# Kernel optimization log

Hardware: AMD Instinct MI355X
Metric: run time of the kernel (lower is better)

The kernel has to match this reference:

```python
import jax, jax.numpy as jnp
import numpy as np

B, IN_DIM, HV_DIM, NUM_CLASSES = 16384, 2048, 8192, 1000


def setup_inputs() -> dict:
    key = jax.random.key(0)
    kx, kp, kc = jax.random.split(key, 3)
    x = jax.random.normal(kx, (B, IN_DIM), dtype=jnp.float32)
    # +/-1 random projection and class hypervectors (2*bernoulli - 1), as in the torch buffers
    proj = (jax.random.randint(kp, (IN_DIM, HV_DIM), 0, 2) * 2 - 1).astype(jnp.float32)
    class_hv = (jax.random.randint(kc, (HV_DIM, NUM_CLASSES), 0, 2) * 2 - 1).astype(jnp.float32)
    return {"x": x, "proj": proj, "class_hv": class_hv}


def reference(x, proj, class_hv):
    # dense projection -> sign binarize -> binary associative-memory matmul (score_mode='dot')
    hv = x @ proj                                   # [B, HV_DIM]
    hv_bin = jnp.where(hv >= 0, 1.0, -1.0).astype(hv.dtype)
    scores = hv_bin @ class_hv                      # [B, NUM_CLASSES]
    return scores, hv_bin
```

## Files before the change

kernel.cpp:

```cpp
#include <hip/hip_runtime.h>
#include <hip/hip_bf16.h>

typedef _Float16 half8  __attribute__((ext_vector_type(8)));
typedef _Float16 half4_t __attribute__((ext_vector_type(4)));
typedef float    floatx4 __attribute__((ext_vector_type(4)));
typedef int      intx4   __attribute__((ext_vector_type(4)));

#define B_DIM   16384
#define IN_D    2048
#define HV_D    8192
#define NC      1000
#define NCP     1024
#define SCORES_N (B_DIM * NC)

#define GLD16(gp, lp) __builtin_amdgcn_global_load_lds( \
    (const __attribute__((address_space(1))) void*)(gp), \
    (__attribute__((address_space(3))) void*)(lp), 16, 0, 0)

__global__ void k_split(const float* __restrict__ x, _Float16* __restrict__ xh) {
    size_t i = (size_t)blockIdx.x * 256 + threadIdx.x;
    floatx4 v = ((const floatx4*)x)[i];
    half4_t h;
#pragma unroll
    for (int j = 0; j < 4; ++j) h[j] = (_Float16)v[j];
    ((half4_t*)xh)[i] = h;
}

__global__ void k_transpose_proj(const float* __restrict__ p, _Float16* __restrict__ pT) {
    __shared__ float tile[64][65];
    const int t = threadIdx.x;
    const int nt = blockIdx.x * 64;
    const int kt = blockIdx.y * 64;
    const int tr = t >> 4, tc = (t & 15) * 4;
#pragma unroll
    for (int s = 0; s < 4; ++s) {
        int r = tr + s * 16;
        floatx4 v = *(const floatx4*)&p[(size_t)(kt + r) * HV_D + nt + tc];
        tile[r][tc] = v[0]; tile[r][tc + 1] = v[1];
        tile[r][tc + 2] = v[2]; tile[r][tc + 3] = v[3];
    }
    __syncthreads();
#pragma unroll
    for (int s = 0; s < 4; ++s) {
        int rn = tr + s * 16;
        half4_t o;
#pragma unroll
        for (int j = 0; j < 4; ++j) o[j] = (_Float16)tile[tc + j][rn];
        *(half4_t*)&pT[(size_t)(nt + rn) * IN_D + kt + tc] = o;
    }
}

__global__ void k_pack_class(const float* __restrict__ c, signed char* __restrict__ cT) {
    __shared__ signed char tile[64][68];
    const int t = threadIdx.x;
    const int nt = blockIdx.x * 64;
    const int kt = blockIdx.y * 64;
    const int nl = t & 63;
    const int n = nt + nl;
#pragma unroll
    for (int s = 0; s < 16; ++s) {
        const int kl = s * 4 + (t >> 6);
        signed char v = 0;
        if (n < NC) {
            float f = c[(size_t)(kt + kl) * NC + n];
            v = (f >= 0.f) ? (signed char)1 : (signed char)-1;
        }
        tile[kl][nl] = v;
    }
    __syncthreads();
    const int wn = t >> 2;
    const int wk = (t & 3) * 16;
    intx4 o;
    signed char* ob = (signed char*)&o;
#pragma unroll
    for (int j = 0; j < 16; ++j) ob[j] = tile[wk + j][wn];
    *(intx4*)&cT[(size_t)(nt + wn) * HV_D + kt + wk] = o;
}

__launch_bounds__(256, 2)
__global__ void k_gemm1(const _Float16* __restrict__ xh,
                        const _Float16* __restrict__ pT,
                        float* __restrict__ hv_out, signed char* __restrict__ hvb,
                        int mbase) {
    __shared__ _Float16 sAh[2][128 * 64];
    __shared__ _Float16 sB [256 * 64];
    const int t = threadIdx.x;
    const int w = t >> 6, l = t & 63;
    const int m0 = mbase + blockIdx.y * 128, n0 = blockIdx.x * 256;
    const int wm = (w >> 1) * 64, wn = (w & 1) * 128;
    const int lm = l & 15, kq = l >> 4;
    const int srow  = w * 8 + (l >> 3);
    const int scol  = (((l & 7) ^ ((l >> 3) & 7))) * 8;
    const int sbyte = w * 1024 + l * 16;

    floatx4 acc[4][8] = {};

    for (int k0 = 0; k0 < IN_D; k0 += 64) {
        __syncthreads();
#pragma unroll
        for (int i = 0; i < 4; ++i) {
            const size_t ga = (size_t)(m0 + srow + i * 32) * IN_D + k0 + scol;
            GLD16(xh + ga, (char*)&sAh[0][0] + sbyte + i * 4096);
        }
#pragma unroll
        for (int i = 0; i < 8; ++i) {
            const size_t gb = (size_t)(n0 + srow + i * 32) * IN_D + k0 + scol;
            GLD16(pT + gb, (char*)sB + sbyte + i * 4096);
        }
        __syncthreads();
#pragma unroll
        for (int ks = 0; ks < 2; ++ks) {
            const int csw = ((ks * 4 + kq) ^ (lm & 7)) * 8;
            half8 b[8];
#pragma unroll
            for (int ns = 0; ns < 8; ++ns)
                b[ns] = *(const half8*)&sB[(wn + ns * 16 + lm) * 64 + csw];
#pragma unroll
            for (int ms = 0; ms < 4; ++ms) {
                half8 a = *(const half8*)&sAh[0][(wm + ms * 16 + lm) * 64 + csw];
#pragma unroll
                for (int ns = 0; ns < 8; ++ns)
                    acc[ms][ns] = __builtin_amdgcn_mfma_f32_16x16x32_f16(a, b[ns], acc[ms][ns], 0, 0, 0);
            }
        }
    }

#pragma unroll
    for (int ms = 0; ms < 4; ++ms) {
#pragma unroll
        for (int ns = 0; ns < 8; ++ns) {
            const int m = m0 + wm + ms * 16 + kq * 4;
            const int n = n0 + wn + ns * 16 + lm;
#pragma unroll
            for (int r = 0; r < 4; ++r) {
                const int pos = (acc[ms][ns][r] >= 0.f);
                const size_t o = (size_t)(m + r) * HV_D + n;
                hv_out[o] = pos ? 1.f : -1.f;
                hvb[o] = (signed char)(pos ? 1 : -1);
            }
        }
    }
}

__launch_bounds__(256, 2)
__global__ void k_gemm2(const signed char* __restrict__ hvb, const signed char* __restrict__ cT,
                        float* __restrict__ scores) {
    __shared__ signed char sA[2][64 * 128];
    __shared__ signed char sB[2][256 * 128];
    const int t = threadIdx.x;
    const int w = t >> 6, l = t & 63;

    const int orig = blockIdx.y * 4 + blockIdx.x;
    const int lid  = (orig & 7) * 128 + (orig >> 3);
    const int bx = lid & 3, by = lid >> 2;

    const int m0 = by * 64, n0 = bx * 256;
    const int wm = (w >> 1) * 32, wn = (w & 1) * 128;
    const int lm = l & 15, kq = l >> 4;
    const int srow  = w * 8 + (l >> 3);
    const int scol  = (((l & 7) ^ ((l >> 3) & 7))) * 16;
    const int sbyte = w * 1024 + l * 16;

    intx4 acc[2][8] = {};

#define G2_STAGE(buf, kt) do { \
    const int k0_ = (kt) * 128; \
    _Pragma("unroll") \
    for (int i = 0; i < 2; ++i) \
        GLD16(hvb + (size_t)(m0 + srow + i * 32) * HV_D + k0_ + scol, \
              (char*)&sA[buf][0] + sbyte + i * 4096); \
    _Pragma("unroll") \
    for (int i = 0; i < 8; ++i) \
        GLD16(cT + (size_t)(n0 + srow + i * 32) * HV_D + k0_ + scol, \
              (char*)&sB[buf][0] + sbyte + i * 4096); \
} while (0)

#define G2_COMPUTE(buf) do { \
    _Pragma("unroll") \
    for (int ks = 0; ks < 2; ++ks) { \
        const int csw = ((ks * 4 + kq) ^ (lm & 7)) * 16; \
        intx4 b[8]; \
        _Pragma("unroll") \
        for (int ns = 0; ns < 8; ++ns) \
            b[ns] = *(const intx4*)&sB[buf][(wn + ns * 16 + lm) * 128 + csw]; \
        _Pragma("unroll") \
        for (int ms = 0; ms < 2; ++ms) { \
            intx4 a = *(const intx4*)&sA[buf][(wm + ms * 16 + lm) * 128 + csw]; \
            _Pragma("unroll") \
            for (int ns = 0; ns < 8; ++ns) \
                acc[ms][ns] = __builtin_amdgcn_mfma_i32_16x16x64_i8(a, b[ns], acc[ms][ns], 0, 0, 0); \
        } \
    } \
} while (0)

    G2_STAGE(0, 0);

#pragma unroll 1
    for (int kt = 0; kt < 63; ++kt) {
        const int cur = kt & 1;
        __builtin_amdgcn_s_barrier();
        if (cur == 0) G2_STAGE(1, kt + 1); else G2_STAGE(0, kt + 1);
        asm volatile("s_waitcnt vmcnt(10)" ::: "memory");
        __builtin_amdgcn_sched_barrier(0);
        __builtin_amdgcn_s_barrier();
        __builtin_amdgcn_sched_barrier(0);
        if (cur == 0) G2_COMPUTE(0); else G2_COMPUTE(1);
    }
    __builtin_amdgcn_s_barrier();
    asm volatile("s_waitcnt vmcnt(0)" ::: "memory");
    __builtin_amdgcn_sched_barrier(0);
    __builtin_amdgcn_s_barrier();
    __builtin_amdgcn_sched_barrier(0);
    G2_COMPUTE(1);

#undef G2_STAGE
#undef G2_COMPUTE

#pragma unroll
    for (int ms = 0; ms < 2; ++ms) {
#pragma unroll
        for (int ns = 0; ns < 8; ++ns) {
            const int m = m0 + wm + ms * 16 + kq * 4;
            const int n = n0 + wn + ns * 16 + lm;
            if (n < NC) {
#pragma unroll
                for (int r = 0; r < 4; ++r)
                    __builtin_nontemporal_store((float)acc[ms][ns][r],
                                                &scores[(size_t)(m + r) * NC + n]);
            }
        }
    }
}

extern "C" void kernel_launch(void* const* d_in, const int* in_sizes, int n_in,
                              void* d_out, int out_size, void* d_ws, size_t ws_size,
                              hipStream_t stream) {
    const float* x    = (const float*)d_in[0];
    const float* proj = (const float*)d_in[1];
    const float* chv  = (const float*)d_in[2];
    float* out    = (float*)d_out;
    float* scores = out;
    float* hv_out = out + (size_t)SCORES_N;

    char* ws = (char*)d_ws;
    _Float16*    xh  = (_Float16*)(ws);
    _Float16*    pT  = (_Float16*)(ws + (size_t)134217728);
    signed char* cT  = (signed char*)(ws + (size_t)167772160);
    signed char* hvb = (signed char*)(ws + (size_t)176160768);

    k_split<<<(B_DIM * IN_D / 4) / 256, 256, 0, stream>>>(x, xh);
    k_transpose_proj<<<dim3(HV_D / 64, IN_D / 64), 256, 0, stream>>>(proj, pT);
    k_pack_class<<<dim3(NCP / 64, HV_D / 64), 256, 0, stream>>>(chv, cT);
    k_gemm1<<<dim3(HV_D / 256, B_DIM / 256), 256, 0, stream>>>(xh, pT, hv_out, hvb, 0);
    k_gemm1<<<dim3(HV_D / 256, B_DIM / 256), 256, 0, stream>>>(xh, pT, hv_out, hvb, B_DIM / 2);
    k_gemm2<<<dim3(NCP / 256, B_DIM / 64), 256, 0, stream>>>(hvb, cT, scores);
}
```

Measured before the change: 1.410 ms.

## Double-buffer GEMM1 shared-memory tiles with async prefetch overlapping MFMA compute

Rewrites the projection GEMM main loop into a two-stage software pipeline. The K tile shrinks from 64 to 32, and two shared buffers each for A and B are used. The next K tile is issued via global_load_lds before the MFMA work on the current tile, with explicit vmcnt waits and raw barriers. The aim is to hide global-memory latency behind MFMA work instead of serializing load and compute each iteration. It also adds an unused 32 KB padding array, kept alive by a never-true branch, which raises per-block LDS use and so caps how many blocks share a CU. The cost is more barriers per unit of K work and a hand-tuned wait count that must stay in step with the number of loads.

```diff
diff --git a/kernel.cpp b/kernel.cpp
--- a/kernel.cpp
+++ b/kernel.cpp
@@ -82,48 +82,68 @@
                         const _Float16* __restrict__ pT,
                         float* __restrict__ hv_out, signed char* __restrict__ hvb,
                         int mbase) {
-    __shared__ _Float16 sAh[2][128 * 64];
-    __shared__ _Float16 sB [256 * 64];
+    __shared__ _Float16 sA[2][128 * 32];
+    __shared__ _Float16 sB[2][256 * 32];
+    __shared__ _Float16 sPad[16384];
     const int t = threadIdx.x;
     const int w = t >> 6, l = t & 63;
     const int m0 = mbase + blockIdx.y * 128, n0 = blockIdx.x * 256;
     const int wm = (w >> 1) * 64, wn = (w & 1) * 128;
     const int lm = l & 15, kq = l >> 4;
-    const int srow  = w * 8 + (l >> 3);
-    const int scol  = (((l & 7) ^ ((l >> 3) & 7))) * 8;
-    const int sbyte = w * 1024 + l * 16;
+    const int srow  = t >> 2;
+    const int gcol  = ((t & 3) ^ ((t >> 3) & 3)) * 8;
+    const int sbyte = t * 16;
+    const int csw   = (kq ^ ((lm >> 1) & 3)) * 8;
+    if ((size_t)hv_out == 1) sPad[0] = (_Float16)0;
 
     floatx4 acc[4][8] = {};
 
-    for (int k0 = 0; k0 < IN_D; k0 += 64) {
-        __syncthreads();
-#pragma unroll
-        for (int i = 0; i < 4; ++i) {
-            const size_t ga = (size_t)(m0 + srow + i * 32) * IN_D + k0 + scol;
-            GLD16(xh + ga, (char*)&sAh[0][0] + sbyte + i * 4096);
-        }
-#pragma unroll
-        for (int i = 0; i < 8; ++i) {
-            const size_t gb = (size_t)(n0 + srow + i * 32) * IN_D + k0 + scol;
-            GLD16(pT + gb, (char*)sB + sbyte + i * 4096);
-        }
-        __syncthreads();
-#pragma unroll
-        for (int ks = 0; ks < 2; ++ks) {
-            const int csw = ((ks * 4 + kq) ^ (lm & 7)) * 8;
-            half8 b[8];
-#pragma unroll
-            for (int ns = 0; ns < 8; ++ns)
-                b[ns] = *(const half8*)&sB[(wn + ns * 16 + lm) * 64 + csw];
-#pragma unroll
-            for (int ms = 0; ms < 4; ++ms) {
-                half8 a = *(const half8*)&sAh[0][(wm + ms * 16 + lm) * 64 + csw];
-#pragma unroll
-                for (int ns = 0; ns < 8; ++ns)
-                    acc[ms][ns] = __builtin_amdgcn_mfma_f32_16x16x32_f16(a, b[ns], acc[ms][ns], 0, 0, 0);
-            }
-        }
-    }
+#define G1_STAGE(buf, kt) do { \
+    const size_t k0_ = (size_t)((kt) * 32 + gcol); \
+    GLD16(xh + (size_t)(m0 + srow)       * IN_D + k0_, (char*)&sA[buf][0] + sbyte); \
+    GLD16(xh + (size_t)(m0 + 64 + srow)  * IN_D + k0_, (char*)&sA[buf][0] + 4096 + sbyte); \
+    GLD16(pT + (size_t)(n0 + srow)       * IN_D + k0_, (char*)&sB[buf][0] + sbyte); \
+    GLD16(pT + (size_t)(n0 + 64 + srow)  * IN_D + k0_, (char*)&sB[buf][0] + 4096 + sbyte); \
+    GLD16(pT + (size_t)(n0 + 128 + srow) * IN_D + k0_, (char*)&sB[buf][0] + 8192 + sbyte); \
+    GLD16(pT + (size_t)(n0 + 192 + srow) * IN_D + k0_, (char*)&sB[buf][0] + 12288 + sbyte); \
+} while (0)
+
+#define G1_COMPUTE(buf) do { \
+    half8 b[8]; \
+    _Pragma("unroll") \
+    for (int ns = 0; ns < 8; ++ns) \
+        b[ns] = *(const half8*)&sB[buf][(wn + ns * 16 + lm) * 32 + csw]; \
+    _Pragma("unroll") \
+    for (int ms = 0; ms < 4; ++ms) { \
+        half8 a = *(const half8*)&sA[buf][(wm + ms * 16 + lm) * 32 + csw]; \
+        _Pragma("unroll") \
+        for (int ns = 0; ns < 8; ++ns) \
+            acc[ms][ns] = __builtin_amdgcn_mfma_f32_16x16x32_f16(a, b[ns], acc[ms][ns], 0, 0, 0); \
+    } \
+} while (0)
+
+    G1_STAGE(0, 0);
+
+#pragma unroll 1
+    for (int kt = 0; kt < 63; ++kt) {
+        const int cur = kt & 1;
+        __builtin_amdgcn_s_barrier();
+        if (cur == 0) G1_STAGE(1, kt + 1); else G1_STAGE(0, kt + 1);
+        asm volatile("s_waitcnt vmcnt(6)" ::: "memory");
+        __builtin_amdgcn_sched_barrier(0);
+        __builtin_amdgcn_s_barrier();
+        __builtin_amdgcn_sched_barrier(0);
+        if (cur == 0) G1_COMPUTE(0); else G1_COMPUTE(1);
+    }
+    __builtin_amdgcn_s_barrier();
+    asm volatile("s_waitcnt vmcnt(0)" ::: "memory");
+    __builtin_amdgcn_sched_barrier(0);
+    __builtin_amdgcn_s_barrier();
+    __builtin_amdgcn_sched_barrier(0);
+    G1_COMPUTE(1);
+
+#undef G1_STAGE
+#undef G1_COMPUTE
 
 #pragma unroll
     for (int ms = 0; ms < 4; ++ms) {
```

Result: slower. 3.238 ms (+129.7%).
